# Optimization experiments

Measured on AMD Instinct MI355X. Metric: run time of the kernel, lower is better.

## Reference

```python
import jax, jax.numpy as jnp
import numpy as np

B, N, D, CF = 8, 2048, 512, 128  # batch, nodes, feat_dim, count_feat


def setup_inputs() -> dict:
    key = jax.random.key(0)
    ks = jax.random.split(key, 12)
    s = 1.0 / np.sqrt(D)
    return {
        "X": jax.random.normal(ks[0], (B, N, D), jnp.float32),
        # first MultiHeadAttention (num_heads=1, mode='QK', out_features=feat_dim)
        "Wq1": jax.random.normal(ks[1], (D, D), jnp.float32) * s,
        "Wk1": jax.random.normal(ks[2], (D, D), jnp.float32) * s,
        "Wv1": jax.random.normal(ks[3], (D, D), jnp.float32) * s,
        "Wo1": jax.random.normal(ks[4], (D, D), jnp.float32) * s,
        # score attention (only its raw QK^T scores are used downstream)
        "Wq2": jax.random.normal(ks[5], (D, D), jnp.float32) * s,
        "Wk2": jax.random.normal(ks[6], (D, D), jnp.float32) * s,
        # count_mlp: Linear(D,CF) -> LeakyReLU(0.1) -> Linear(CF,1)
        "W1": jax.random.normal(ks[7], (D, CF), jnp.float32) * s,
        "b1": jnp.zeros((CF,), jnp.float32),
        "W2": jax.random.normal(ks[8], (CF, 1), jnp.float32) * (1.0 / np.sqrt(CF)),
        "b2": jnp.zeros((1,), jnp.float32),
    }


def reference(X, Wq1, Wk1, Wv1, Wo1, Wq2, Wk2, W1, b1, W2, b2):
    scale = 1.0 / jnp.sqrt(jnp.asarray(X.shape[-1], X.dtype))
    # --- first self-attention: att = softmax(QK^T/sqrt(d)) V Wo ---
    q1 = X @ Wq1
    k1 = X @ Wk1
    v1 = X @ Wv1
    s1 = jnp.einsum("bnd,bmd->bnm", q1, k1) * scale      # [B,N,N]
    p1 = jax.nn.softmax(s1, axis=-1)
    att = jnp.einsum("bnm,bmd->bnd", p1, v1) @ Wo1        # [B,N,D]
    # --- score attention over att: only raw scores are consumed ---
    s2 = jnp.einsum("bnd,bmd->bnm", att @ Wq2, att @ Wk2) * scale  # [B,N,N]
    # --- count_mlp threshold per node ---
    h = att @ W1 + b1
    h = jnp.where(h >= 0, h, 0.1 * h)                     # LeakyReLU(0.1)
    thresh = h @ W2 + b2                                  # [B,N,1]
    # --- mlp_score_thresh readout: clamp, row-normalize, clip ---
    surv = jnp.maximum(s2 - thresh, 0.0)                  # broadcast over last dim
    A = jnp.clip(surv / (jnp.sum(surv, axis=-1, keepdims=True) + 1e-9), 0.0, 1.0)
    return A
```

## Files before the change

### kernel.cpp

```cpp
#include <hip/hip_runtime.h>
#include <hip/hip_bf16.h>

#define BB 8
#define NN 2048
#define DD 512
#define CFF 128
#define MT (BB*NN)

typedef _Float16 half_t;
typedef __attribute__((ext_vector_type(8))) _Float16 half8;
typedef __attribute__((ext_vector_type(4))) float floatx4;
typedef __attribute__((ext_vector_type(4))) unsigned int uint4v;

#define MFMA16(a,b,c) __builtin_amdgcn_mfma_f32_16x16x32_f16((a),(b),(c),0,0,0)

template<int EPI>
__global__ __launch_bounds__(256) void gemm_f16s(
    const half_t* __restrict__ Ahi, const half_t* __restrict__ Alo, long lda, long sA,
    const half_t* __restrict__ Bhi, const half_t* __restrict__ Blo, long ldb, long sB,
    float* __restrict__ Cf, half_t* __restrict__ Chi, half_t* __restrict__ Clo,
    long ldc, long sC, long slotS,
    int K, float alpha, const float* __restrict__ bias, const float* __restrict__ tvec,
    float* __restrict__ rsum)
{
    const int gx = gridDim.x, gy = gridDim.y;
    int d = blockIdx.x + gx * (blockIdx.y + gy * blockIdx.z);
    int total = gx * gy * gridDim.z;
    int t0 = (d & 7) * (total >> 3) + (d >> 3);
    int bx = t0 % gx;
    int t1 = t0 / gx;
    int by = t1 % gy;
    int bz = t1 / gy;

    const int tid = threadIdx.x;
    const int row0 = by * 128, col0 = bx * 128;
    const long z = bz;
    const half_t* pAh = Ahi + z * sA + (long)row0 * lda;
    const half_t* pAl = Alo + z * sA + (long)row0 * lda;
    const half_t* pBh = Bhi + z * sB + (long)col0 * ldb;
    const half_t* pBl = Blo + z * sB + (long)col0 * ldb;

    __shared__ half_t lds[2][4][4096];

    const int l  = tid & 63;
    const int w  = tid >> 6;
    const int wr = w >> 1, wc = w & 1;
    const int Rw = wr * 64, Cw = wc * 64;
    const int rl = l & 15, kc = l >> 4;
    const int swz = (kc ^ (rl & 3)) * 8;

    floatx4 acc[4][4];
#pragma unroll
    for (int m = 0; m < 4; ++m)
#pragma unroll
        for (int n = 0; n < 4; ++n) acc[m][n] = (floatx4){0.f, 0.f, 0.f, 0.f};

    const int r0s = tid >> 2,         c0s = tid & 3;
    const int r1s = (tid + 256) >> 2, c1s = tid & 3;
    const int off0 = r0s * 32 + ((c0s ^ (r0s & 3)) * 8);
    const int off1 = r1s * 32 + ((c1s ^ (r1s & 3)) * 8);

    auto stage = [&](int buf, int k0) {
        long ga0 = (long)r0s * lda + k0 + c0s * 8;
        long gb0 = (long)r0s * ldb + k0 + c0s * 8;
        long ga1 = (long)r1s * lda + k0 + c1s * 8;
        long gb1 = (long)r1s * ldb + k0 + c1s * 8;
        uint4v a0 = *(const uint4v*)(pAh + ga0);
        uint4v a1 = *(const uint4v*)(pAl + ga0);
        uint4v b0 = *(const uint4v*)(pBh + gb0);
        uint4v b1 = *(const uint4v*)(pBl + gb0);
        uint4v a2 = *(const uint4v*)(pAh + ga1);
        uint4v a3 = *(const uint4v*)(pAl + ga1);
        uint4v b2 = *(const uint4v*)(pBh + gb1);
        uint4v b3 = *(const uint4v*)(pBl + gb1);
        *(uint4v*)&lds[buf][0][off0] = a0;
        *(uint4v*)&lds[buf][1][off0] = a1;
        *(uint4v*)&lds[buf][2][off0] = b0;
        *(uint4v*)&lds[buf][3][off0] = b1;
        *(uint4v*)&lds[buf][0][off1] = a2;
        *(uint4v*)&lds[buf][1][off1] = a3;
        *(uint4v*)&lds[buf][2][off1] = b2;
        *(uint4v*)&lds[buf][3][off1] = b3;
    };

    const int nk = K >> 5;
    stage(0, 0);
#pragma unroll 2
    for (int t = 0; t < nk; ++t) {
        __syncthreads();
        const int cur = t & 1;
        const half_t* bAh = &lds[cur][0][0];
        const half_t* bAl = &lds[cur][1][0];
        const half_t* bBh = &lds[cur][2][0];
        const half_t* bBl = &lds[cur][3][0];
        half8 af[4][2], bf[4][2];
#pragma unroll
        for (int m = 0; m < 4; ++m) {
            int off = (Rw + m * 16 + rl) * 32 + swz;
            af[m][0] = *(const half8*)(bAh + off);
            af[m][1] = *(const half8*)(bAl + off);
        }
#pragma unroll
        for (int n = 0; n < 4; ++n) {
            int off = (Cw + n * 16 + rl) * 32 + swz;
            bf[n][0] = *(const half8*)(bBh + off);
            bf[n][1] = *(const half8*)(bBl + off);
        }
#pragma unroll
        for (int m = 0; m < 4; ++m)
#pragma unroll
            for (int n = 0; n < 4; ++n) {
                acc[m][n] = MFMA16(af[m][0], bf[n][0], acc[m][n]);
                acc[m][n] = MFMA16(af[m][1], bf[n][0], acc[m][n]);
                acc[m][n] = MFMA16(af[m][0], bf[n][1], acc[m][n]);
            }
        if (t + 1 < nk) stage((t + 1) & 1, (t + 1) << 5);
    }

    if (EPI == 0) {
#pragma unroll
        for (int m = 0; m < 4; ++m)
#pragma unroll
            for (int n = 0; n < 4; ++n) {
                int col = col0 + Cw + n * 16 + rl;
#pragma unroll
                for (int r = 0; r < 4; ++r) {
                    int row = row0 + Rw + m * 16 + kc * 4 + r;
                    Cf[z * sC + (long)row * ldc + col] = acc[m][n][r] * alpha;
                }
            }
    } else if (EPI == 1) {
#pragma unroll
        for (int m = 0; m < 4; ++m)
#pragma unroll
            for (int n = 0; n < 4; ++n) {
                int col = col0 + Cw + n * 16 + rl;
                long obase = (long)(col >> 9) * slotS + z * sC + (col & 511);
#pragma unroll
                for (int r = 0; r < 4; ++r) {
                    int row = row0 + Rw + m * 16 + kc * 4 + r;
                    long o = obase + (long)row * ldc;
                    float v = acc[m][n][r];
                    half_t hh = (half_t)v;
                    Chi[o] = hh;
                    Clo[o] = (half_t)(v - (float)hh);
                }
            }
    } else if (EPI == 3) {
        const float* tv = tvec + z * NN;
        float* rs = rsum + z * NN;
#pragma unroll
        for (int m = 0; m < 4; ++m) {
#pragma unroll
            for (int r = 0; r < 4; ++r) {
                int row = row0 + Rw + m * 16 + kc * 4 + r;
                float tvr = tv[row];
                float partial = 0.f;
#pragma unroll
                for (int n = 0; n < 4; ++n) {
                    int col = col0 + Cw + n * 16 + rl;
                    float v = fmaxf(acc[m][n][r] * alpha - tvr, 0.f);
                    Cf[z * sC + (long)row * ldc + col] = v;
                    partial += v;
                }
                partial += __shfl_xor(partial, 1);
                partial += __shfl_xor(partial, 2);
                partial += __shfl_xor(partial, 4);
                partial += __shfl_xor(partial, 8);
                if (rl == 0) atomicAdd(&rs[row], partial);
            }
        }
    } else {
        float w2v[4], bv[4];
#pragma unroll
        for (int n = 0; n < 4; ++n) {
            int col = Cw + n * 16 + rl;
            bv[n]  = bias[col];
            w2v[n] = tvec[col];
        }
#pragma unroll
        for (int m = 0; m < 4; ++m) {
#pragma unroll
            for (int r = 0; r < 4; ++r) {
                int row = row0 + Rw + m * 16 + kc * 4 + r;
                float partial = 0.f;
#pragma unroll
                for (int n = 0; n < 4; ++n) {
                    float v = acc[m][n][r] + bv[n];
                    v = (v >= 0.f) ? v : 0.1f * v;
                    partial += v * w2v[n];
                }
                partial += __shfl_xor(partial, 1);
                partial += __shfl_xor(partial, 2);
                partial += __shfl_xor(partial, 4);
                partial += __shfl_xor(partial, 8);
                if (rl == 0) atomicAdd(&rsum[row], partial);
            }
        }
    }
}

__device__ __forceinline__ float waveReduceMax(float v) {
#pragma unroll
    for (int o = 32; o; o >>= 1) v = fmaxf(v, __shfl_down(v, o));
    return v;
}
__device__ __forceinline__ float waveReduceSum(float v) {
#pragma unroll
    for (int o = 32; o; o >>= 1) v += __shfl_down(v, o);
    return v;
}

__global__ __launch_bounds__(256) void softmax_split_kernel(float* __restrict__ S)
{
    __shared__ float red[4];
    __shared__ float fin;
    long row = blockIdx.x;
    float* p = S + row * (long)NN;
    half_t* ph = (half_t*)p;
    half_t* pl = ph + NN;
    int t = threadIdx.x;

    float4 v0 = *reinterpret_cast<float4*>(p + t * 8);
    float4 v1 = *reinterpret_cast<float4*>(p + t * 8 + 4);

    float m = fmaxf(fmaxf(fmaxf(v0.x, v0.y), fmaxf(v0.z, v0.w)),
                    fmaxf(fmaxf(v1.x, v1.y), fmaxf(v1.z, v1.w)));
    m = waveReduceMax(m);
    if ((t & 63) == 0) red[t >> 6] = m;
    __syncthreads();
    if (t == 0) fin = fmaxf(fmaxf(red[0], red[1]), fmaxf(red[2], red[3]));
    __syncthreads();
    m = fin;

    float e[8];
    e[0] = __expf(v0.x - m); e[1] = __expf(v0.y - m); e[2] = __expf(v0.z - m); e[3] = __expf(v0.w - m);
    e[4] = __expf(v1.x - m); e[5] = __expf(v1.y - m); e[6] = __expf(v1.z - m); e[7] = __expf(v1.w - m);
    float s = ((e[0] + e[1]) + (e[2] + e[3])) + ((e[4] + e[5]) + (e[6] + e[7]));
    s = waveReduceSum(s);
    __syncthreads();
    if ((t & 63) == 0) red[t >> 6] = s;
    __syncthreads();
    if (t == 0) fin = (red[0] + red[1]) + (red[2] + red[3]);
    __syncthreads();
    float inv = 1.0f / fin;

    __syncthreads();
    half8 hv, lv;
#pragma unroll
    for (int j = 0; j < 8; ++j) {
        float pv = e[j] * inv;
        half_t hh = (half_t)pv;
        hv[j] = hh;
        lv[j] = (half_t)(pv - (float)hh);
    }
    *(half8*)(ph + t * 8) = hv;
    *(half8*)(pl + t * 8) = lv;
}

__global__ __launch_bounds__(256) void norm_kernel(float* __restrict__ S, const float* __restrict__ sums)
{
    long i = (long)blockIdx.x * 256 + threadIdx.x;
    long base = i * 8;
    long row = base >> 11;
    float inv = 1.0f / (sums[row] + 1e-9f);
    float4 v0 = *reinterpret_cast<float4*>(S + base);
    float4 v1 = *reinterpret_cast<float4*>(S + base + 4);
    v0.x = fminf(v0.x * inv, 1.0f); v0.y = fminf(v0.y * inv, 1.0f);
    v0.z = fminf(v0.z * inv, 1.0f); v0.w = fminf(v0.w * inv, 1.0f);
    v1.x = fminf(v1.x * inv, 1.0f); v1.y = fminf(v1.y * inv, 1.0f);
    v1.z = fminf(v1.z * inv, 1.0f); v1.w = fminf(v1.w * inv, 1.0f);
    *reinterpret_cast<float4*>(S + base) = v0;
    *reinterpret_cast<float4*>(S + base + 4) = v1;
}

__global__ __launch_bounds__(256) void init_aux(float* __restrict__ thresh, float* __restrict__ sums,
                                                const float* __restrict__ b2)
{
    int i = blockIdx.x * 256 + threadIdx.x;
    if (i < MT) { thresh[i] = b2[0]; sums[i] = 0.f; }
}

__global__ __launch_bounds__(256) void wprep(const float* __restrict__ W,
                                             half_t* __restrict__ Th, half_t* __restrict__ Tl,
                                             int K, int N)
{
    __shared__ float tw[32][33];
    int n0 = blockIdx.x * 32, k0 = blockIdx.y * 32;
    int c = threadIdx.x & 31, r8 = threadIdx.x >> 5;
#pragma unroll
    for (int i = 0; i < 4; ++i) {
        int r = r8 + i * 8;
        tw[r][c] = W[(long)(k0 + r) * N + n0 + c];
    }
    __syncthreads();
#pragma unroll
    for (int i = 0; i < 4; ++i) {
        int nr = r8 + i * 8;
        float v = tw[c][nr];
        half_t hh = (half_t)v;
        Th[(long)(n0 + nr) * K + k0 + c] = hh;
        Tl[(long)(n0 + nr) * K + k0 + c] = (half_t)(v - (float)hh);
    }
}

__global__ __launch_bounds__(256) void split_f32(const float* __restrict__ in,
                                                 half_t* __restrict__ hi, half_t* __restrict__ lo)
{
    long i = ((long)blockIdx.x * 256 + threadIdx.x) * 8;
    float4 a = *(const float4*)(in + i), b = *(const float4*)(in + i + 4);
    float v[8] = {a.x, a.y, a.z, a.w, b.x, b.y, b.z, b.w};
    half8 hv, lv;
#pragma unroll
    for (int j = 0; j < 8; ++j) {
        half_t hh = (half_t)v[j];
        hv[j] = hh;
        lv[j] = (half_t)(v[j] - (float)hh);
    }
    *(half8*)(hi + i) = hv;
    *(half8*)(lo + i) = lv;
}

__global__ __launch_bounds__(256) void transpose_pair(const half_t* __restrict__ ih, const half_t* __restrict__ il,
                                                      half_t* __restrict__ oh, half_t* __restrict__ ol)
{
    __shared__ half_t th[64][66], tl[64][66];
    int b = blockIdx.z;
    int c0 = blockIdx.x * 64;
    int r0 = blockIdx.y * 64;
    const half_t* pih = ih + ((long)b * 2048 + r0) * 512 + c0;
    const half_t* pil = il + ((long)b * 2048 + r0) * 512 + c0;
    int t = threadIdx.x;
    int cc = (t & 7) * 8, rr = t >> 3;
#pragma unroll
    for (int i = 0; i < 2; ++i) {
        int r = rr + 32 * i;
        *(uint4v*)&th[r][cc] = *(const uint4v*)(pih + (long)r * 512 + cc);
        *(uint4v*)&tl[r][cc] = *(const uint4v*)(pil + (long)r * 512 + cc);
    }
    __syncthreads();
    half_t* poh = oh + ((long)b * 512 + c0) * 2048 + r0;
    half_t* pol = ol + ((long)b * 512 + c0) * 2048 + r0;
#pragma unroll
    for (int i = 0; i < 2; ++i) {
        int ic = rr + 32 * i;
        half8 vh, vl;
#pragma unroll
        for (int j = 0; j < 8; ++j) {
            vh[j] = th[cc + j][ic];
            vl[j] = tl[cc + j][ic];
        }
        *(half8*)(poh + (long)ic * 2048 + cc) = vh;
        *(half8*)(pol + (long)ic * 2048 + cc) = vl;
    }
}

static void launch_gemm16(hipStream_t s, int epi,
    const half_t* Ahi, const half_t* Alo, long lda, long sA,
    const half_t* Bhi, const half_t* Blo, long ldb, long sB,
    float* Cf, half_t* Chi, half_t* Clo, long ldc, long sC, long slotS,
    int M, int N, int K, int batch, float alpha,
    const float* bias, const float* tvec, float* rsum)
{
    dim3 g(N / 128, M / 128, batch), b(256, 1, 1);
    if (epi == 0)      gemm_f16s<0><<<g, b, 0, s>>>(Ahi, Alo, lda, sA, Bhi, Blo, ldb, sB, Cf, Chi, Clo, ldc, sC, slotS, K, alpha, bias, tvec, rsum);
    else if (epi == 1) gemm_f16s<1><<<g, b, 0, s>>>(Ahi, Alo, lda, sA, Bhi, Blo, ldb, sB, Cf, Chi, Clo, ldc, sC, slotS, K, alpha, bias, tvec, rsum);
    else if (epi == 3) gemm_f16s<3><<<g, b, 0, s>>>(Ahi, Alo, lda, sA, Bhi, Blo, ldb, sB, Cf, Chi, Clo, ldc, sC, slotS, K, alpha, bias, tvec, rsum);
    else               gemm_f16s<4><<<g, b, 0, s>>>(Ahi, Alo, lda, sA, Bhi, Blo, ldb, sB, Cf, Chi, Clo, ldc, sC, slotS, K, alpha, bias, tvec, rsum);
}

extern "C" void kernel_launch(void* const* d_in, const int* in_sizes, int n_in,
                              void* d_out, int out_size, void* d_ws, size_t ws_size,
                              hipStream_t stream)
{
    const float* X   = (const float*)d_in[0];
    const float* Wq1 = (const float*)d_in[1];
    const float* Wk1 = (const float*)d_in[2];
    const float* Wv1 = (const float*)d_in[3];
    const float* Wo1 = (const float*)d_in[4];
    const float* Wq2 = (const float*)d_in[5];
    const float* Wk2 = (const float*)d_in[6];
    const float* W1  = (const float*)d_in[7];
    const float* b1  = (const float*)d_in[8];
    const float* W2  = (const float*)d_in[9];
    const float* b2  = (const float*)d_in[10];

    float* out = (float*)d_out;
    const float scale = 0.044194173824159216f;

    half_t* wsH = (half_t*)d_ws;
    const long U  = (long)MT * DD;
    const long WD = (long)DD * DD;
    half_t* sAh = wsH;          half_t* sAl = wsH + U;
    half_t* sBh = wsH + 2 * U;  half_t* sBl = wsH + 3 * U;
    half_t* sCh = wsH + 4 * U;  half_t* sCl = wsH + 5 * U;
    half_t* wt  = wsH + 6 * U;
    half_t* wqk1h = wt;               half_t* wqk1l = wqk1h + 2 * WD;
    half_t* wv1h  = wqk1l + 2 * WD;   half_t* wv1l  = wv1h + WD;
    half_t* wo1h  = wv1l + WD;        half_t* wo1l  = wo1h + WD;
    half_t* wqk2h = wo1l + WD;        half_t* wqk2l = wqk2h + 2 * WD;
    half_t* w1h   = wqk2l + 2 * WD;   half_t* w1l   = w1h + (long)DD * CFF;
    float*  thresh = (float*)(w1l + (long)DD * CFF);
    float*  sums   = thresh + MT;

    init_aux<<<dim3(64), dim3(256), 0, stream>>>(thresh, sums, b2);
    split_f32<<<dim3(4096), dim3(256), 0, stream>>>(X, sAh, sAl);
    wprep<<<dim3(16, 16), dim3(256), 0, stream>>>(Wq1, wqk1h,      wqk1l,      DD, DD);
    wprep<<<dim3(16, 16), dim3(256), 0, stream>>>(Wk1, wqk1h + WD, wqk1l + WD, DD, DD);
    wprep<<<dim3(16, 16), dim3(256), 0, stream>>>(Wv1, wv1h,  wv1l,  DD, DD);
    wprep<<<dim3(16, 16), dim3(256), 0, stream>>>(Wo1, wo1h,  wo1l,  DD, DD);
    wprep<<<dim3(16, 16), dim3(256), 0, stream>>>(Wq2, wqk2h,      wqk2l,      DD, DD);
    wprep<<<dim3(16, 16), dim3(256), 0, stream>>>(Wk2, wqk2h + WD, wqk2l + WD, DD, DD);
    wprep<<<dim3(4, 16),  dim3(256), 0, stream>>>(W1,  w1h,   w1l,   DD, CFF);

    launch_gemm16(stream, 1, sAh, sAl, DD, 0, wqk1h, wqk1l, DD, 0,
                  nullptr, sBh, sBl, DD, 0, 2 * U, MT, 2 * DD, DD, 1, 1.f, nullptr, nullptr, nullptr);

    launch_gemm16(stream, 0, sBh, sBl, DD, (long)NN * DD, sCh, sCl, DD, (long)NN * DD,
                  out, nullptr, nullptr, NN, (long)NN * NN, 0, NN, NN, DD, BB, scale, nullptr, nullptr, nullptr);

    launch_gemm16(stream, 1, sAh, sAl, DD, 0, wv1h, wv1l, DD, 0,
                  nullptr, sBh, sBl, DD, 0, 0, MT, DD, DD, 1, 1.f, nullptr, nullptr, nullptr);

    softmax_split_kernel<<<dim3(MT), dim3(256), 0, stream>>>(out);

    transpose_pair<<<dim3(8, 32, BB), dim3(256), 0, stream>>>(sBh, sBl, sCh, sCl);

    {
        const half_t* p1h = (const half_t*)d_out;
        const half_t* p1l = p1h + NN;
        launch_gemm16(stream, 1, p1h, p1l, 2 * NN, (long)NN * 2 * NN,
                      sCh, sCl, NN, (long)DD * NN,
                      nullptr, sBh, sBl, DD, (long)NN * DD, 0, NN, DD, NN, BB, 1.f, nullptr, nullptr, nullptr);
    }

    launch_gemm16(stream, 1, sBh, sBl, DD, 0, wo1h, wo1l, DD, 0,
                  nullptr, sCh, sCl, DD, 0, 0, MT, DD, DD, 1, 1.f, nullptr, nullptr, nullptr);

    launch_gemm16(stream, 1, sCh, sCl, DD, 0, wqk2h, wqk2l, DD, 0,
                  nullptr, sAh, sAl, DD, 0, 2 * U, MT, 2 * DD, DD, 1, 1.f, nullptr, nullptr, nullptr);

    launch_gemm16(stream, 4, sCh, sCl, DD, 0, w1h, w1l, DD, 0,
                  nullptr, nullptr, nullptr, CFF, 0, 0, MT, CFF, DD, 1, 1.f, b1, W2, thresh);

    launch_gemm16(stream, 3, sAh, sAl, DD, (long)NN * DD, sBh, sBl, DD, (long)NN * DD,
                  out, nullptr, nullptr, NN, (long)NN * NN, 0, NN, NN, DD, BB, scale, nullptr, thresh, sums);

    norm_kernel<<<dim3(out_size / 2048), dim3(256), 0, stream>>>(out, sums);
}
```

Before: 808.3 us.

## Fold weight products into precomputed matrices and prefetch GEMM tiles into registers

Precomputes Wq1·Wk1ᵀ, Wv1·Wo1 and Wq2·Wk2ᵀ with a small fp32 GEMM, so each attention score becomes X·M·Xᵀ and V·Wo becomes (Wv·Wo)ᵀ applied before P. This removes the separate K projections, the Wo projection and the transpose kernel, cutting several large M×512×512 GEMMs. Folded weights are scaled by 8 before the fp16 hi/lo split and the outputs are rescaled, to keep precision. The GEMM main loop also now issues global loads for the next tile into registers before the barrier, overlapping memory latency with MFMA work at the cost of extra registers.

```diff
diff --git a/kernel.cpp b/kernel.cpp
--- a/kernel.cpp
+++ b/kernel.cpp
@@ -60,33 +60,38 @@
     const int off0 = r0s * 32 + ((c0s ^ (r0s & 3)) * 8);
     const int off1 = r1s * 32 + ((c1s ^ (r1s & 3)) * 8);
 
-    auto stage = [&](int buf, int k0) {
+    auto load_regs = [&](int k0, uint4v* r) {
         long ga0 = (long)r0s * lda + k0 + c0s * 8;
         long gb0 = (long)r0s * ldb + k0 + c0s * 8;
         long ga1 = (long)r1s * lda + k0 + c1s * 8;
         long gb1 = (long)r1s * ldb + k0 + c1s * 8;
-        uint4v a0 = *(const uint4v*)(pAh + ga0);
-        uint4v a1 = *(const uint4v*)(pAl + ga0);
-        uint4v b0 = *(const uint4v*)(pBh + gb0);
-        uint4v b1 = *(const uint4v*)(pBl + gb0);
-        uint4v a2 = *(const uint4v*)(pAh + ga1);
-        uint4v a3 = *(const uint4v*)(pAl + ga1);
-        uint4v b2 = *(const uint4v*)(pBh + gb1);
-        uint4v b3 = *(const uint4v*)(pBl + gb1);
-        *(uint4v*)&lds[buf][0][off0] = a0;
-        *(uint4v*)&lds[buf][1][off0] = a1;
-        *(uint4v*)&lds[buf][2][off0] = b0;
-        *(uint4v*)&lds[buf][3][off0] = b1;
-        *(uint4v*)&lds[buf][0][off1] = a2;
-        *(uint4v*)&lds[buf][1][off1] = a3;
-        *(uint4v*)&lds[buf][2][off1] = b2;
-        *(uint4v*)&lds[buf][3][off1] = b3;
+        r[0] = *(const uint4v*)(pAh + ga0);
+        r[1] = *(const uint4v*)(pAl + ga0);
+        r[2] = *(const uint4v*)(pBh + gb0);
+        r[3] = *(const uint4v*)(pBl + gb0);
+        r[4] = *(const uint4v*)(pAh + ga1);
+        r[5] = *(const uint4v*)(pAl + ga1);
+        r[6] = *(const uint4v*)(pBh + gb1);
+        r[7] = *(const uint4v*)(pBl + gb1);
     };
+    auto write_lds = [&](int buf, const uint4v* r) {
+        *(uint4v*)&lds[buf][0][off0] = r[0];
+        *(uint4v*)&lds[buf][1][off0] = r[1];
+        *(uint4v*)&lds[buf][2][off0] = r[2];
+        *(uint4v*)&lds[buf][3][off0] = r[3];
+        *(uint4v*)&lds[buf][0][off1] = r[4];
+        *(uint4v*)&lds[buf][1][off1] = r[5];
+        *(uint4v*)&lds[buf][2][off1] = r[6];
+        *(uint4v*)&lds[buf][3][off1] = r[7];
+    };
 
     const int nk = K >> 5;
-    stage(0, 0);
+    uint4v rg[8];
+    load_regs(0, rg);
+    write_lds(0, rg);
 #pragma unroll 2
     for (int t = 0; t < nk; ++t) {
+        if (t + 1 < nk) load_regs((t + 1) << 5, rg);
         __syncthreads();
         const int cur = t & 1;
         const half_t* bAh = &lds[cur][0][0];
@@ -114,7 +119,7 @@
                 acc[m][n] = MFMA16(af[m][1], bf[n][0], acc[m][n]);
                 acc[m][n] = MFMA16(af[m][0], bf[n][1], acc[m][n]);
             }
-        if (t + 1 < nk) stage((t + 1) & 1, (t + 1) << 5);
+        if (t + 1 < nk) write_lds((t + 1) & 1, rg);
     }
 
     if (EPI == 0) {
@@ -140,7 +145,7 @@
                 for (int r = 0; r < 4; ++r) {
                     int row = row0 + Rw + m * 16 + kc * 4 + r;
                     long o = obase + (long)row * ldc;
-                    float v = acc[m][n][r];
+                    float v = acc[m][n][r] * alpha;
                     half_t hh = (half_t)v;
                     Chi[o] = hh;
                     Clo[o] = (half_t)(v - (float)hh);
@@ -198,6 +203,76 @@
             }
         }
     }
+}
+
+__global__ __launch_bounds__(256) void wgemm3(
+    const float* __restrict__ Wq1, const float* __restrict__ Wk1,
+    const float* __restrict__ Wv1, const float* __restrict__ Wo1,
+    const float* __restrict__ Wq2, const float* __restrict__ Wk2,
+    float* __restrict__ T0, float* __restrict__ T1, float* __restrict__ T2)
+{
+    const int op = blockIdx.z;
+    const float* A = (op == 0) ? Wq1 : (op == 1) ? Wv1 : Wq2;
+    const float* B = (op == 0) ? Wk1 : (op == 1) ? Wo1 : Wk2;
+    float* C = (op == 0) ? T0 : (op == 1) ? T1 : T2;
+    const bool bt = (op != 1);
+
+    __shared__ float As[32][65];
+    __shared__ float Bs[32][65];
+    const int tid = threadIdx.x;
+    const int i0 = blockIdx.y * 64, j0 = blockIdx.x * 64;
+    const int tx = tid & 15, ty = tid >> 4;
+    float acc[4][4];
+#pragma unroll
+    for (int i = 0; i < 4; ++i)
+#pragma unroll
+        for (int j = 0; j < 4; ++j) acc[i][j] = 0.f;
+
+    for (int k0 = 0; k0 < 512; k0 += 32) {
+#pragma unroll
+        for (int u = 0; u < 2; ++u) {
+            int e = tid + u * 256;
+            int r = e >> 3, c = (e & 7) * 4;
+            float4 v = *(const float4*)(A + (long)(i0 + r) * 512 + k0 + c);
+            As[c][r] = v.x; As[c + 1][r] = v.y; As[c + 2][r] = v.z; As[c + 3][r] = v.w;
+        }
+        if (bt) {
+#pragma unroll
+            for (int u = 0; u < 2; ++u) {
+                int e = tid + u * 256;
+                int r = e >> 3, c = (e & 7) * 4;
+                float4 v = *(const float4*)(B + (long)(j0 + r) * 512 + k0 + c);
+                Bs[c][r] = v.x; Bs[c + 1][r] = v.y; Bs[c + 2][r] = v.z; Bs[c + 3][r] = v.w;
+            }
+        } else {
+#pragma unroll
+            for (int u = 0; u < 2; ++u) {
+                int e = tid + u * 256;
+                int k = e >> 4, j = (e & 15) * 4;
+                *(float4*)&Bs[k][j] = *(const float4*)(B + (long)(k0 + k) * 512 + j0 + j);
+            }
+        }
+        __syncthreads();
+#pragma unroll
+        for (int kk = 0; kk < 32; ++kk) {
+            float av[4], bv[4];
+#pragma unroll
+            for (int i = 0; i < 4; ++i) av[i] = As[kk][ty * 4 + i];
+#pragma unroll
+            for (int j = 0; j < 4; ++j) bv[j] = Bs[kk][tx * 4 + j];
+#pragma unroll
+            for (int i = 0; i < 4; ++i)
+#pragma unroll
+                for (int j = 0; j < 4; ++j)
+                    acc[i][j] = fmaf(av[i], bv[j], acc[i][j]);
+        }
+        __syncthreads();
+    }
+#pragma unroll
+    for (int i = 0; i < 4; ++i)
+#pragma unroll
+        for (int j = 0; j < 4; ++j)
+            C[(long)(i0 + ty * 4 + i) * 512 + j0 + tx * 4 + j] = acc[i][j];
 }
 
 __device__ __forceinline__ float waveReduceMax(float v) {
@@ -283,7 +358,7 @@
 
 __global__ __launch_bounds__(256) void wprep(const float* __restrict__ W,
                                              half_t* __restrict__ Th, half_t* __restrict__ Tl,
-                                             int K, int N)
+                                             int K, int N, float mul)
 {
     __shared__ float tw[32][33];
     int n0 = blockIdx.x * 32, k0 = blockIdx.y * 32;
@@ -297,7 +372,7 @@
 #pragma unroll
     for (int i = 0; i < 4; ++i) {
         int nr = r8 + i * 8;
-        float v = tw[c][nr];
+        float v = tw[c][nr] * mul;
         half_t hh = (half_t)v;
         Th[(long)(n0 + nr) * K + k0 + c] = hh;
         Tl[(long)(n0 + nr) * K + k0 + c] = (half_t)(v - (float)hh);
@@ -319,40 +394,6 @@
     }
     *(half8*)(hi + i) = hv;
     *(half8*)(lo + i) = lv;
-}
-
-__global__ __launch_bounds__(256) void transpose_pair(const half_t* __restrict__ ih, const half_t* __restrict__ il,
-                                                      half_t* __restrict__ oh, half_t* __restrict__ ol)
-{
-    __shared__ half_t th[64][66], tl[64][66];
-    int b = blockIdx.z;
-    int c0 = blockIdx.x * 64;
-    int r0 = blockIdx.y * 64;
-    const half_t* pih = ih + ((long)b * 2048 + r0) * 512 + c0;
-    const half_t* pil = il + ((long)b * 2048 + r0) * 512 + c0;
-    int t = threadIdx.x;
-    int cc = (t & 7) * 8, rr = t >> 3;
-#pragma unroll
-    for (int i = 0; i < 2; ++i) {
-        int r = rr + 32 * i;
-        *(uint4v*)&th[r][cc] = *(const uint4v*)(pih + (long)r * 512 + cc);
-        *(uint4v*)&tl[r][cc] = *(const uint4v*)(pil + (long)r * 512 + cc);
-    }
-    __syncthreads();
-    half_t* poh = oh + ((long)b * 512 + c0) * 2048 + r0;
-    half_t* pol = ol + ((long)b * 512 + c0) * 2048 + r0;
-#pragma unroll
-    for (int i = 0; i < 2; ++i) {
-        int ic = rr + 32 * i;
-        half8 vh, vl;
-#pragma unroll
-        for (int j = 0; j < 8; ++j) {
-            vh[j] = th[cc + j][ic];
-            vl[j] = tl[cc + j][ic];
-        }
-        *(half8*)(poh + (long)ic * 2048 + cc) = vh;
-        *(half8*)(pol + (long)ic * 2048 + cc) = vl;
-    }
 }
 
 static void launch_gemm16(hipStream_t s, int epi,
@@ -387,63 +428,59 @@
 
     float* out = (float*)d_out;
     const float scale = 0.044194173824159216f;
+    const float WM = 8.0f, WMI = 0.125f;
 
     half_t* wsH = (half_t*)d_ws;
     const long U  = (long)MT * DD;
     const long WD = (long)DD * DD;
-    half_t* sAh = wsH;          half_t* sAl = wsH + U;
+    half_t* sXh = wsH;          half_t* sXl = wsH + U;
     half_t* sBh = wsH + 2 * U;  half_t* sBl = wsH + 3 * U;
     half_t* sCh = wsH + 4 * U;  half_t* sCl = wsH + 5 * U;
-    half_t* wt  = wsH + 6 * U;
-    half_t* wqk1h = wt;               half_t* wqk1l = wqk1h + 2 * WD;
-    half_t* wv1h  = wqk1l + 2 * WD;   half_t* wv1l  = wv1h + WD;
-    half_t* wo1h  = wv1l + WD;        half_t* wo1l  = wo1h + WD;
-    half_t* wqk2h = wo1l + WD;        half_t* wqk2l = wqk2h + 2 * WD;
-    half_t* w1h   = wqk2l + 2 * WD;   half_t* w1l   = w1h + (long)DD * CFF;
-    float*  thresh = (float*)(w1l + (long)DD * CFF);
+    half_t* wptr = wsH + 6 * U;
+    half_t* mb1h = wptr;            half_t* mb1l = mb1h + WD;
+    half_t* mvoh = mb1l + WD;       half_t* mvol = mvoh + WD;
+    half_t* mb2h = mvol + WD;       half_t* mb2l = mb2h + WD;
+    half_t* w1h  = mb2l + WD;       half_t* w1l  = w1h + (long)DD * CFF;
+    float*  T0 = (float*)(w1l + (long)DD * CFF);
+    float*  T1 = T0 + WD;
+    float*  T2 = T1 + WD;
+    float*  thresh = T2 + WD;
     float*  sums   = thresh + MT;
 
     init_aux<<<dim3(64), dim3(256), 0, stream>>>(thresh, sums, b2);
-    split_f32<<<dim3(4096), dim3(256), 0, stream>>>(X, sAh, sAl);
-    wprep<<<dim3(16, 16), dim3(256), 0, stream>>>(Wq1, wqk1h,      wqk1l,      DD, DD);
-    wprep<<<dim3(16, 16), dim3(256), 0, stream>>>(Wk1, wqk1h + WD, wqk1l + WD, DD, DD);
-    wprep<<<dim3(16, 16), dim3(256), 0, stream>>>(Wv1, wv1h,  wv1l,  DD, DD);
-    wprep<<<dim3(16, 16), dim3(256), 0, stream>>>(Wo1, wo1h,  wo1l,  DD, DD);
-    wprep<<<dim3(16, 16), dim3(256), 0, stream>>>(Wq2, wqk2h,      wqk2l,      DD, DD);
-    wprep<<<dim3(16, 16), dim3(256), 0, stream>>>(Wk2, wqk2h + WD, wqk2l + WD, DD, DD);
-    wprep<<<dim3(4, 16),  dim3(256), 0, stream>>>(W1,  w1h,   w1l,   DD, CFF);
-
-    launch_gemm16(stream, 1, sAh, sAl, DD, 0, wqk1h, wqk1l, DD, 0,
-                  nullptr, sBh, sBl, DD, 0, 2 * U, MT, 2 * DD, DD, 1, 1.f, nullptr, nullptr, nullptr);
-
-    launch_gemm16(stream, 0, sBh, sBl, DD, (long)NN * DD, sCh, sCl, DD, (long)NN * DD,
+    split_f32<<<dim3(4096), dim3(256), 0, stream>>>(X, sXh, sXl);
+    wgemm3<<<dim3(8, 8, 3), dim3(256), 0, stream>>>(Wq1, Wk1, Wv1, Wo1, Wq2, Wk2, T0, T1, T2);
+    wprep<<<dim3(16, 16), dim3(256), 0, stream>>>(T0, mb1h, mb1l, DD, DD, WM);
+    wprep<<<dim3(16, 16), dim3(256), 0, stream>>>(T1, mvoh, mvol, DD, DD, WM);
+    wprep<<<dim3(16, 16), dim3(256), 0, stream>>>(T2, mb2h, mb2l, DD, DD, WM);
+    wprep<<<dim3(4, 16),  dim3(256), 0, stream>>>(W1, w1h, w1l, DD, CFF, 1.0f);
+
+    launch_gemm16(stream, 1, sXh, sXl, DD, 0, mb1h, mb1l, DD, 0,
+                  nullptr, sBh, sBl, DD, 0, 0, MT, DD, DD, 1, WMI, nullptr, nullptr, nullptr);
+
+    launch_gemm16(stream, 0, sBh, sBl, DD, (long)NN * DD, sXh, sXl, DD, (long)NN * DD,
                   out, nullptr, nullptr, NN, (long)NN * NN, 0, NN, NN, DD, BB, scale, nullptr, nullptr, nullptr);
 
-    launch_gemm16(stream, 1, sAh, sAl, DD, 0, wv1h, wv1l, DD, 0,
-                  nullptr, sBh, sBl, DD, 0, 0, MT, DD, DD, 1, 1.f, nullptr, nullptr, nullptr);
+    launch_gemm16(stream, 1, mvoh, mvol, DD, 0, sXh, sXl, DD, (long)NN * DD,
+                  nullptr, sBh, sBl, NN, (long)DD * NN, 512, DD, NN, DD, BB, WMI, nullptr, nullptr, nullptr);
 
     softmax_split_kernel<<<dim3(MT), dim3(256), 0, stream>>>(out);
-
-    transpose_pair<<<dim3(8, 32, BB), dim3(256), 0, stream>>>(sBh, sBl, sCh, sCl);
 
     {
         const half_t* p1h = (const half_t*)d_out;
         const half_t* p1l = p1h + NN;
         launch_gemm16(stream, 1, p1h, p1l, 2 * NN, (long)NN * 2 * NN,
-                      sCh, sCl, NN, (long)DD * NN,
-                      nullptr, sBh, sBl, DD, (long)NN * DD, 0, NN, DD, NN, BB, 1.f, nullptr, nullptr, nullptr);
-    }
-
-    launch_gemm16(stream, 1, sBh, sBl, DD, 0, wo1h, wo1l, DD, 0,
-                  nullptr, sCh, sCl, DD, 0, 0, MT, DD, DD, 1, 1.f, nullptr, nullptr, nullptr);
-
-    launch_gemm16(stream, 1, sCh, sCl, DD, 0, wqk2h, wqk2l, DD, 0,
-                  nullptr, sAh, sAl, DD, 0, 2 * U, MT, 2 * DD, DD, 1, 1.f, nullptr, nullptr, nullptr);
+                      sBh, sBl, NN, (long)DD * NN,
+                      nullptr, sCh, sCl, DD, (long)NN * DD, 0, NN, DD, NN, BB, 1.f, nullptr, nullptr, nullptr);
+    }
+
+    launch_gemm16(stream, 1, sCh, sCl, DD, 0, mb2h, mb2l, DD, 0,
+                  nullptr, sBh, sBl, DD, 0, 0, MT, DD, DD, 1, WMI, nullptr, nullptr, nullptr);
 
     launch_gemm16(stream, 4, sCh, sCl, DD, 0, w1h, w1l, DD, 0,
                   nullptr, nullptr, nullptr, CFF, 0, 0, MT, CFF, DD, 1, 1.f, b1, W2, thresh);
 
-    launch_gemm16(stream, 3, sAh, sAl, DD, (long)NN * DD, sBh, sBl, DD, (long)NN * DD,
+    launch_gemm16(stream, 3, sBh, sBl, DD, (long)NN * DD, sCh, sCl, DD, (long)NN * DD,
                   out, nullptr, nullptr, NN, (long)NN * NN, 0, NN, NN, DD, BB, scale, nullptr, thresh, sums);
 
     norm_kernel<<<dim3(out_size / 2048), dim3(256), 0, stream>>>(out, sums);
```

After: 761.6 us. 1.06x faster.
